# Kernel optimization log

Measured on AMD Instinct MI355X. Metric: run time of the kernel, lower is better.

Reference implementation:

```python
import jax, jax.numpy as jnp
import numpy as np

H = 64  # LSTM units for both layers
T = 128  # sequence length
D = 128  # input feature dim
B = 2048  # batch

def setup_inputs() -> dict:
    key = jax.random.key(0)
    ks = jax.random.split(key, 7)
    s_in = 1.0 / np.sqrt(D)
    s_h = 1.0 / np.sqrt(H)
    return {
        "x": jax.random.normal(ks[0], (B, T, D), dtype=jnp.float32),
        # Keras LSTM weights: kernel [in, 4H], recurrent_kernel [H, 4H], bias [4H]
        # gate order: i, f, g (cell candidate), o
        "W1": jax.random.normal(ks[1], (D, 4 * H), dtype=jnp.float32) * s_in,
        "U1": jax.random.normal(ks[2], (H, 4 * H), dtype=jnp.float32) * s_h,
        "b1": jnp.zeros((4 * H,), dtype=jnp.float32),
        "W2": jax.random.normal(ks[3], (H, 4 * H), dtype=jnp.float32) * s_h,
        "U2": jax.random.normal(ks[4], (H, 4 * H), dtype=jnp.float32) * s_h,
        "b2": jnp.zeros((4 * H,), dtype=jnp.float32),
    }

def _lstm(x, W, U, b, act):
    """Keras-faithful LSTM, return_sequences=True, zero init state.
    x: [B, T, D_in] -> hs: [B, T, H]
    recurrent_activation = sigmoid; `act` is the cell/output activation.
    """
    Bsz = x.shape[0]
    # Precompute input projections for all timesteps (one big GEMM).
    xz = jnp.einsum('btd,dg->btg', x, W) + b  # [B, T, 4H]
    xz = jnp.swapaxes(xz, 0, 1)  # [T, B, 4H]

    def step(carry, zt):
        h, c = carry
        z = zt + h @ U  # [B, 4H]
        i, f, g, o = jnp.split(z, 4, axis=-1)
        i = jax.nn.sigmoid(i)
        f = jax.nn.sigmoid(f)
        g = act(g)
        o = jax.nn.sigmoid(o)
        c = f * c + i * g
        h = o * act(c)
        return (h, c), h

    init = (jnp.zeros((Bsz, H), x.dtype), jnp.zeros((Bsz, H), x.dtype))
    _, hs = jax.lax.scan(step, init, xz)  # hs: [T, B, H]
    return jnp.swapaxes(hs, 0, 1)  # [B, T, H]

def reference(x, W1, U1, b1, W2, U2, b2):
    h1 = _lstm(x, W1, U1, b1, jnp.tanh)           # layer 1: default tanh
    h2 = _lstm(h1, W2, U2, b2, jax.nn.sigmoid)    # layer 2: activation='sigmoid'
    return h2.reshape(h2.shape[0], T * H, 1)      # Reshape((8192, 1))
```

## Files before the change

### kernel.cpp

```cpp
#include <hip/hip_runtime.h>
#include <stdint.h>

typedef __attribute__((ext_vector_type(8))) short short8;
typedef __attribute__((ext_vector_type(4))) short short4_t;
typedef __attribute__((ext_vector_type(4))) float floatx4;

#define TT 128
#define DD 128

__device__ __forceinline__ short f2bf(float f) {
  union { float f; uint32_t u; } v; v.f = f;
  uint32_t u = v.u;
  u += 0x7fffu + ((u >> 16) & 1u);
  return (short)(u >> 16);
}

__device__ __forceinline__ float sigf(float x) {
  return __builtin_amdgcn_rcpf(1.f + __expf(-x));
}
__device__ __forceinline__ float tanhf_(float x) {
  return 2.f * __builtin_amdgcn_rcpf(1.f + __expf(-2.f * x)) - 1.f;
}

__global__ void wtrans_all(const float* __restrict__ W1, const float* __restrict__ U1,
                           const float* __restrict__ W2, const float* __restrict__ U2,
                           short* __restrict__ w1t, short* __restrict__ u1t,
                           short* __restrict__ w2t, short* __restrict__ u2t) {
  int n = blockIdx.x;
  int k = threadIdx.x;
  w1t[n * 128 + k] = f2bf(W1[k * 256 + n]);
  if (k < 64) {
    u1t[n * 64 + k] = f2bf(U1[k * 256 + n]);
    w2t[n * 64 + k] = f2bf(W2[k * 256 + n]);
    u2t[n * 64 + k] = f2bf(U2[k * 256 + n]);
  }
}

__global__ __launch_bounds__(256, 1) void lstm_fused(
    const float* __restrict__ x,
    const short* __restrict__ w1t, const short* __restrict__ u1t,
    const short* __restrict__ w2t, const short* __restrict__ u2t,
    const float* __restrict__ b1, const float* __restrict__ b2,
    float* __restrict__ out) {
  __shared__ short hb1[8 * 64];
  __shared__ short hb2[8 * 64];
  __shared__ short xbuf[8 * 128];

  const int tid = threadIdx.x;
  const int w = tid >> 6;
  const int lane = tid & 63;
  const int mrow = lane & 15;
  const int quad = lane >> 4;
  const int rowbase = blockIdx.x * 8;
  const int colw = w * 16 + mrow;
  const int br_a = 2 * (mrow >> 2) + (mrow & 1);

  short8 w1r[4][4], u1r[4][2], w2r[4][2], u2r[4][2];
#pragma unroll
  for (int g = 0; g < 4; ++g) {
    const int n = g * 4 + w;
#pragma unroll
    for (int s = 0; s < 4; ++s)
      w1r[g][s] = *(const short8*)(w1t + n * 2048 + mrow * 128 + quad * 8 + s * 32);
#pragma unroll
    for (int s = 0; s < 2; ++s) {
      u1r[g][s] = *(const short8*)(u1t + n * 1024 + mrow * 64 + quad * 8 + s * 32);
      w2r[g][s] = *(const short8*)(w2t + n * 1024 + mrow * 64 + quad * 8 + s * 32);
      u2r[g][s] = *(const short8*)(u2t + n * 1024 + mrow * 64 + quad * 8 + s * 32);
    }
  }
  float bias1[4], bias2[4];
#pragma unroll
  for (int g = 0; g < 4; ++g) {
    bias1[g] = b1[g * 64 + colw];
    bias2[g] = b2[g * 64 + colw];
  }

  const int xr = tid >> 5;
  const int dgrp = tid & 31;
  const float* xload = x + (size_t)(rowbase + xr) * (TT * DD) + dgrp * 4;
  const int cbx = dgrp >> 1;
  const int px = (cbx & 8) | ((cbx ^ xr) & 7);
  short* xwr = &xbuf[xr * 128 + px * 8 + (dgrp & 1) * 4];

  short8 h1f[2], h2f[2];
  float c1[2] = {0.f, 0.f}, c2[2] = {0.f, 0.f};
#pragma unroll
  for (int s = 0; s < 2; ++s)
#pragma unroll
    for (int j = 0; j < 8; ++j) { h1f[s][j] = 0; h2f[s][j] = 0; }

  {
    floatx4 x0 = *(const floatx4*)(xload);
    short4_t v;
#pragma unroll
    for (int j = 0; j < 4; ++j) v[j] = f2bf(x0[j]);
    *(short4_t*)xwr = v;
  }
  __syncthreads();
  short8 xf[4];
#pragma unroll
  for (int s = 0; s < 4; ++s) {
    int cb = quad + 4 * s;
    int p = (cb & 8) | ((cb ^ br_a) & 7);
    xf[s] = *(const short8*)&xbuf[br_a * 128 + p * 8];
  }
  __syncthreads();
  floatx4 xraw = *(const floatx4*)(xload + DD);

#pragma unroll 1
  for (int t = 0; t < TT; ++t) {
    floatx4 acc[4];
#pragma unroll
    for (int g = 0; g < 4; ++g)
      acc[g] = floatx4{bias1[g], bias1[g], bias1[g], bias1[g]};
#pragma unroll
    for (int g = 0; g < 4; ++g) {
#pragma unroll
      for (int s = 0; s < 4; ++s)
        acc[g] = __builtin_amdgcn_mfma_f32_16x16x32_bf16(xf[s], w1r[g][s], acc[g], 0, 0, 0);
#pragma unroll
      for (int s = 0; s < 2; ++s)
        acc[g] = __builtin_amdgcn_mfma_f32_16x16x32_bf16(h1f[s], u1r[g][s], acc[g], 0, 0, 0);
    }

    {
      short4_t v;
#pragma unroll
      for (int j = 0; j < 4; ++j) v[j] = f2bf(xraw[j]);
      *(short4_t*)xwr = v;
      int tn = (t + 2 < TT) ? t + 2 : TT - 1;
      xraw = *(const floatx4*)(xload + (size_t)tn * DD);
    }

#pragma unroll
    for (int r = 0; r < 2; ++r) {
      float ig = sigf(acc[0][r]);
      float fg = sigf(acc[1][r]);
      float gg = tanhf_(acc[2][r]);
      float og = sigf(acc[3][r]);
      float c = fg * c1[r] + ig * gg;
      c1[r] = c;
      float h = og * tanhf_(c);
      int br = 2 * quad + r;
      int cb = colw >> 3;
      hb1[br * 64 + (((cb ^ br) & 7) << 3) + (colw & 7)] = f2bf(h);
    }
    __syncthreads();
#pragma unroll
    for (int s = 0; s < 2; ++s) {
      int kg = quad + 4 * s;
      h1f[s] = *(const short8*)&hb1[br_a * 64 + (((kg ^ br_a) & 7) << 3)];
    }
#pragma unroll
    for (int s = 0; s < 4; ++s) {
      int cb = quad + 4 * s;
      int p = (cb & 8) | ((cb ^ br_a) & 7);
      xf[s] = *(const short8*)&xbuf[br_a * 128 + p * 8];
    }

    floatx4 bcc[4];
#pragma unroll
    for (int g = 0; g < 4; ++g)
      bcc[g] = floatx4{bias2[g], bias2[g], bias2[g], bias2[g]};
#pragma unroll
    for (int g = 0; g < 4; ++g) {
#pragma unroll
      for (int s = 0; s < 2; ++s)
        bcc[g] = __builtin_amdgcn_mfma_f32_16x16x32_bf16(h1f[s], w2r[g][s], bcc[g], 0, 0, 0);
#pragma unroll
      for (int s = 0; s < 2; ++s)
        bcc[g] = __builtin_amdgcn_mfma_f32_16x16x32_bf16(h2f[s], u2r[g][s], bcc[g], 0, 0, 0);
    }

#pragma unroll
    for (int r = 0; r < 2; ++r) {
      float ig = sigf(bcc[0][r]);
      float fg = sigf(bcc[1][r]);
      float gg = sigf(bcc[2][r]);
      float og = sigf(bcc[3][r]);
      float c = fg * c2[r] + ig * gg;
      c2[r] = c;
      float h = og * sigf(c);
      int br = 2 * quad + r;
      int cb = colw >> 3;
      hb2[br * 64 + (((cb ^ br) & 7) << 3) + (colw & 7)] = f2bf(h);
      out[(size_t)(rowbase + br) * 8192 + t * 64 + colw] = h;
    }
    __syncthreads();
#pragma unroll
    for (int s = 0; s < 2; ++s) {
      int kg = quad + 4 * s;
      h2f[s] = *(const short8*)&hb2[br_a * 64 + (((kg ^ br_a) & 7) << 3)];
    }
  }
}

extern "C" void kernel_launch(void* const* d_in, const int* in_sizes, int n_in,
                              void* d_out, int out_size, void* d_ws, size_t ws_size,
                              hipStream_t stream) {
  const float* x  = (const float*)d_in[0];
  const float* W1 = (const float*)d_in[1];
  const float* U1 = (const float*)d_in[2];
  const float* b1 = (const float*)d_in[3];
  const float* W2 = (const float*)d_in[4];
  const float* U2 = (const float*)d_in[5];
  const float* b2 = (const float*)d_in[6];
  float* out = (float*)d_out;

  short* w1t = (short*)d_ws;
  short* u1t = w1t + 32768;
  short* w2t = u1t + 16384;
  short* u2t = w2t + 16384;

  hipLaunchKernelGGL(wtrans_all, dim3(256), dim3(128), 0, stream,
                     W1, U1, W2, U2, w1t, u1t, w2t, u2t);
  hipLaunchKernelGGL(lstm_fused, dim3(256), dim3(256), 0, stream,
                     x, w1t, u1t, w2t, u2t, b1, b2, out);
}
```

Before: 302.0 us.

## Halve batch rows per block to launch twice the blocks with two per CU

Each block now handles 4 batch rows instead of 8, and the grid doubles to 512 blocks with launch bounds allowing two blocks per CU. The 16-row MFMA tile then carries only 4 distinct rows, so each lane does the gate math for one element instead of two. This shortens the serial per-timestep activation work and spreads blocks over more CUs. In exchange the MFMAs do redundant work, the register budget is tighter for two blocks per CU, and the shared buffers switch from XOR swizzling to padded rows.

```diff
diff --git a/kernel.cpp b/kernel.cpp
--- a/kernel.cpp
+++ b/kernel.cpp
@@ -2,7 +2,7 @@
 #include <stdint.h>
 
 typedef __attribute__((ext_vector_type(8))) short short8;
-typedef __attribute__((ext_vector_type(4))) short short4_t;
+typedef __attribute__((ext_vector_type(2))) short short2_t;
 typedef __attribute__((ext_vector_type(4))) float floatx4;
 
 #define TT 128
@@ -36,24 +36,24 @@
   }
 }
 
-__global__ __launch_bounds__(256, 1) void lstm_fused(
+__global__ __launch_bounds__(256, 2) void lstm_fused(
     const float* __restrict__ x,
     const short* __restrict__ w1t, const short* __restrict__ u1t,
     const short* __restrict__ w2t, const short* __restrict__ u2t,
     const float* __restrict__ b1, const float* __restrict__ b2,
     float* __restrict__ out) {
-  __shared__ short hb1[8 * 64];
-  __shared__ short hb2[8 * 64];
-  __shared__ short xbuf[8 * 128];
+  __shared__ short hb1[4 * 80];
+  __shared__ short hb2[4 * 80];
+  __shared__ short xbuf[4 * 144];
 
   const int tid = threadIdx.x;
   const int w = tid >> 6;
   const int lane = tid & 63;
   const int mrow = lane & 15;
   const int quad = lane >> 4;
-  const int rowbase = blockIdx.x * 8;
+  const int rowbase = blockIdx.x * 4;
   const int colw = w * 16 + mrow;
-  const int br_a = 2 * (mrow >> 2) + (mrow & 1);
+  const int br_a = mrow >> 2;
 
   short8 w1r[4][4], u1r[4][2], w2r[4][2], u2r[4][2];
 #pragma unroll
@@ -76,44 +76,35 @@
     bias2[g] = b2[g * 64 + colw];
   }
 
-  const int xr = tid >> 5;
-  const int dgrp = tid & 31;
-  const float* xload = x + (size_t)(rowbase + xr) * (TT * DD) + dgrp * 4;
-  const int cbx = dgrp >> 1;
-  const int px = (cbx & 8) | ((cbx ^ xr) & 7);
-  short* xwr = &xbuf[xr * 128 + px * 8 + (dgrp & 1) * 4];
+  const int xr = tid >> 6;
+  const int xc = (tid & 63) * 2;
+  const float* xload = x + (size_t)(rowbase + xr) * (TT * DD) + xc;
+  short* xwr = &xbuf[xr * 144 + xc];
 
   short8 h1f[2], h2f[2];
-  float c1[2] = {0.f, 0.f}, c2[2] = {0.f, 0.f};
+  float c1 = 0.f, c2 = 0.f;
 #pragma unroll
   for (int s = 0; s < 2; ++s)
 #pragma unroll
     for (int j = 0; j < 8; ++j) { h1f[s][j] = 0; h2f[s][j] = 0; }
 
   {
-    floatx4 x0 = *(const floatx4*)(xload);
-    short4_t v;
-#pragma unroll
-    for (int j = 0; j < 4; ++j) v[j] = f2bf(x0[j]);
-    *(short4_t*)xwr = v;
+    float a0 = xload[0], a1 = xload[1];
+    *(short2_t*)xwr = short2_t{f2bf(a0), f2bf(a1)};
   }
   __syncthreads();
   short8 xf[4];
 #pragma unroll
-  for (int s = 0; s < 4; ++s) {
-    int cb = quad + 4 * s;
-    int p = (cb & 8) | ((cb ^ br_a) & 7);
-    xf[s] = *(const short8*)&xbuf[br_a * 128 + p * 8];
-  }
+  for (int s = 0; s < 4; ++s)
+    xf[s] = *(const short8*)&xbuf[br_a * 144 + (quad + 4 * s) * 8];
   __syncthreads();
-  floatx4 xraw = *(const floatx4*)(xload + DD);
+  float xr0 = xload[DD], xr1 = xload[DD + 1];
 
 #pragma unroll 1
   for (int t = 0; t < TT; ++t) {
     floatx4 acc[4];
 #pragma unroll
-    for (int g = 0; g < 4; ++g)
-      acc[g] = floatx4{bias1[g], bias1[g], bias1[g], bias1[g]};
+    for (int g = 0; g < 4; ++g) acc[g] = floatx4{0.f, 0.f, 0.f, 0.f};
 #pragma unroll
     for (int g = 0; g < 4; ++g) {
 #pragma unroll
@@ -124,45 +115,34 @@
         acc[g] = __builtin_amdgcn_mfma_f32_16x16x32_bf16(h1f[s], u1r[g][s], acc[g], 0, 0, 0);
     }
 
+    *(short2_t*)xwr = short2_t{f2bf(xr0), f2bf(xr1)};
     {
-      short4_t v;
-#pragma unroll
-      for (int j = 0; j < 4; ++j) v[j] = f2bf(xraw[j]);
-      *(short4_t*)xwr = v;
       int tn = (t + 2 < TT) ? t + 2 : TT - 1;
-      xraw = *(const floatx4*)(xload + (size_t)tn * DD);
+      xr0 = xload[(size_t)tn * DD];
+      xr1 = xload[(size_t)tn * DD + 1];
     }
 
-#pragma unroll
-    for (int r = 0; r < 2; ++r) {
-      float ig = sigf(acc[0][r]);
-      float fg = sigf(acc[1][r]);
-      float gg = tanhf_(acc[2][r]);
-      float og = sigf(acc[3][r]);
-      float c = fg * c1[r] + ig * gg;
-      c1[r] = c;
+    {
+      float ig = sigf(acc[0][0] + bias1[0]);
+      float fg = sigf(acc[1][0] + bias1[1]);
+      float gg = tanhf_(acc[2][0] + bias1[2]);
+      float og = sigf(acc[3][0] + bias1[3]);
+      float c = fg * c1 + ig * gg;
+      c1 = c;
       float h = og * tanhf_(c);
-      int br = 2 * quad + r;
-      int cb = colw >> 3;
-      hb1[br * 64 + (((cb ^ br) & 7) << 3) + (colw & 7)] = f2bf(h);
+      hb1[quad * 80 + colw] = f2bf(h);
     }
     __syncthreads();
 #pragma unroll
-    for (int s = 0; s < 2; ++s) {
-      int kg = quad + 4 * s;
-      h1f[s] = *(const short8*)&hb1[br_a * 64 + (((kg ^ br_a) & 7) << 3)];
-    }
+    for (int s = 0; s < 2; ++s)
+      h1f[s] = *(const short8*)&hb1[br_a * 80 + (quad + 4 * s) * 8];
 #pragma unroll
-    for (int s = 0; s < 4; ++s) {
-      int cb = quad + 4 * s;
-      int p = (cb & 8) | ((cb ^ br_a) & 7);
-      xf[s] = *(const short8*)&xbuf[br_a * 128 + p * 8];
-    }
+    for (int s = 0; s < 4; ++s)
+      xf[s] = *(const short8*)&xbuf[br_a * 144 + (quad + 4 * s) * 8];
 
     floatx4 bcc[4];
 #pragma unroll
-    for (int g = 0; g < 4; ++g)
-      bcc[g] = floatx4{bias2[g], bias2[g], bias2[g], bias2[g]};
+    for (int g = 0; g < 4; ++g) bcc[g] = floatx4{0.f, 0.f, 0.f, 0.f};
 #pragma unroll
     for (int g = 0; g < 4; ++g) {
 #pragma unroll
@@ -173,26 +153,21 @@
         bcc[g] = __builtin_amdgcn_mfma_f32_16x16x32_bf16(h2f[s], u2r[g][s], bcc[g], 0, 0, 0);
     }
 
-#pragma unroll
-    for (int r = 0; r < 2; ++r) {
-      float ig = sigf(bcc[0][r]);
-      float fg = sigf(bcc[1][r]);
-      float gg = sigf(bcc[2][r]);
-      float og = sigf(bcc[3][r]);
-      float c = fg * c2[r] + ig * gg;
-      c2[r] = c;
+    {
+      float ig = sigf(bcc[0][0] + bias2[0]);
+      float fg = sigf(bcc[1][0] + bias2[1]);
+      float gg = sigf(bcc[2][0] + bias2[2]);
+      float og = sigf(bcc[3][0] + bias2[3]);
+      float c = fg * c2 + ig * gg;
+      c2 = c;
       float h = og * sigf(c);
-      int br = 2 * quad + r;
-      int cb = colw >> 3;
-      hb2[br * 64 + (((cb ^ br) & 7) << 3) + (colw & 7)] = f2bf(h);
-      out[(size_t)(rowbase + br) * 8192 + t * 64 + colw] = h;
+      hb2[quad * 80 + colw] = f2bf(h);
+      out[(size_t)(rowbase + quad) * 8192 + t * 64 + colw] = h;
     }
     __syncthreads();
 #pragma unroll
-    for (int s = 0; s < 2; ++s) {
-      int kg = quad + 4 * s;
-      h2f[s] = *(const short8*)&hb2[br_a * 64 + (((kg ^ br_a) & 7) << 3)];
-    }
+    for (int s = 0; s < 2; ++s)
+      h2f[s] = *(const short8*)&hb2[br_a * 80 + (quad + 4 * s) * 8];
   }
 }
 
@@ -215,6 +190,6 @@
 
   hipLaunchKernelGGL(wtrans_all, dim3(256), dim3(128), 0, stream,
                      W1, U1, W2, U2, w1t, u1t, w2t, u2t);
-  hipLaunchKernelGGL(lstm_fused, dim3(256), dim3(256), 0, stream,
+  hipLaunchKernelGGL(lstm_fused, dim3(512), dim3(256), 0, stream,
                      x, w1t, u1t, w2t, u2t, b1, b2, out);
 }
```

Result: faster. 295.7 us (-2.1%).
